# Kernel optimization log

Hardware: AMD Instinct MI355X
Metric: run time of the kernel (lower is better)

Reference implementation:

```python
import jax, jax.numpy as jnp
import numpy as np

N, T, CIN = 40000, 32, 8
VW = 64          # back_voxelwise_channels
P = 16           # v2b_maxvoxels (voxels stacked per BEV cell)
BEV_H, BEV_W = 496, 432
EPS = 1e-5


def _bn(key, shape):
    # returns stacked (gamma, beta, running_mean, running_var) along axis -2
    k1, k2, k3 = jax.random.split(key, 3)
    g = 1.0 + 0.1 * jax.random.normal(k1, shape, jnp.float32)
    b = 0.1 * jax.random.normal(k2, shape, jnp.float32)
    m = 0.1 * jax.random.normal(k3, shape, jnp.float32)
    v = jnp.ones(shape, jnp.float32)
    return jnp.stack([g, b, m, v], axis=-2)


def setup_inputs() -> dict:
    key = jax.random.key(0)
    ks = jax.random.split(key, 20)
    features = jax.random.normal(ks[0], (N, T, CIN), jnp.float32)
    cy = jax.random.randint(ks[1], (N, 1), 0, BEV_H)
    cx = jax.random.randint(ks[2], (N, 1), 0, BEV_W)
    coors = jnp.concatenate([cy, cx], axis=1).astype(jnp.int32)
    num_voxels = jax.random.randint(ks[3], (N,), 1, T + 1).astype(jnp.int32)

    def w(k, o, i):
        return jax.random.normal(k, (o, i), jnp.float32) / float(np.sqrt(i))

    return dict(
        features=features, coors=coors, num_voxels=num_voxels,
        vfe1_W=w(ks[4], 8, CIN), vfe1_bn=_bn(ks[5], (8,)),
        vfe2_W=w(ks[6], 32, 16), vfe2_bn=_bn(ks[7], (32,)),
        vfe3_W=w(ks[8], 64, 64), vfe3_bn=_bn(ks[9], (64,)),
        vfe4_W=w(ks[10], 64, 64), vfe4_bn=_bn(ks[11], (64,)),
        bfe1_W=jax.random.normal(ks[12], (16, P, P), jnp.float32) / float(np.sqrt(P)),
        bfe1_bn=_bn(ks[13], (16, P)),
        bfe2_W=jax.random.normal(ks[14], (16, 2, P), jnp.float32) / float(np.sqrt(P)),
        bfe2_bn=_bn(ks[15], (16, 2)),
        bfe3_W=w(ks[16], 128, 128), bfe3_bn=_bn(ks[17], (128,)),
    )


def _forward(features, vfe1_W, vfe1_bn, vfe2_W, vfe2_bn, vfe3_W, vfe3_bn,
             vfe4_W, vfe4_bn, bfe1_W, bfe1_bn, bfe2_W, bfe2_bn, bfe3_W, bfe3_bn,
             coors, num_voxels):
    n, t = features.shape[0], features.shape[1]
    f32 = features.dtype
    mask = (jnp.arange(t)[None, :] < num_voxels[:, None]).astype(f32)[..., None]  # [N,T,1]

    def fe(x, W, bn):  # Linear (no bias) + BatchNorm1d (eval) + Mish
        g, b, m, v = bn
        y = x @ W.T
        y = (y - m) * jax.lax.rsqrt(v + EPS) * g + b
        return y * jnp.tanh(jax.nn.softplus(y))

    def vfe(x, W, bn):  # pointwise FE, max-pool over points, concat
        p = fe(x, W, bn)
        agg = jnp.max(p, axis=1, keepdims=True)
        return jnp.concatenate([p, jnp.broadcast_to(agg, p.shape)], axis=2)

    x1 = vfe(features, vfe1_W, vfe1_bn)           # [N,T,16]
    x2 = vfe(x1, vfe2_W, vfe2_bn) * mask          # [N,T,64]
    x3 = fe(x2, vfe3_W, vfe3_bn)
    x4 = fe(x3, vfe4_W, vfe4_bn) * mask + x2
    voxelwise = jnp.max(x4, axis=1)               # [N,64]

    # ---- voxel2bev: group voxels by BEV cell, stack up to P per cell ----
    cell = coors[:, 0] * BEV_W + coors[:, 1]                         # [N]
    ucell, inv = jnp.unique(cell, return_inverse=True, size=n, fill_value=BEV_H * BEV_W)
    order = jnp.argsort(inv)                                          # stable
    inv_sorted = inv[order]
    pos_sorted = jnp.arange(n) - jnp.searchsorted(inv_sorted, inv_sorted, side='left')
    slot = jnp.zeros(n, jnp.int32).at[order].set(pos_sorted.astype(jnp.int32))
    row = jnp.where(slot < P, inv, n)                                 # overflow -> dropped
    bevs = jnp.zeros((n, P, VW), f32).at[row, jnp.minimum(slot, P - 1)].set(
        voxelwise, mode='drop')                                       # [N,P,64]
    counts = jax.ops.segment_sum(jnp.ones(n, jnp.int32), inv, num_segments=n)
    numv = jnp.minimum(counts, P)
    bevcoors = jnp.stack([ucell // BEV_W, ucell % BEV_W], axis=1)     # [N,2]

    # ---- 16 grouped FE stacks over the slot dimension ----
    x0 = bevs.transpose(0, 2, 1).reshape(n, 16, 4, P)                 # [N,16,4,P]
    m2 = (jnp.arange(P)[None, :] < numv[:, None]).astype(f32)[:, None, None, :]
    y = jnp.einsum('ngip,gqp->ngiq', x0, bfe1_W)                      # [N,16,4,P]
    g1, b1, m1, v1 = (bfe1_bn[None, :, i, None, :] for i in range(4))
    y = (y - m1) * jax.lax.rsqrt(v1 + EPS) * g1 + b1
    y = y * jnp.tanh(jax.nn.softplus(y)) * m2
    z = jnp.einsum('ngip,gcp->ngic', y, bfe2_W)                       # [N,16,4,2]
    g2, b2, m2b, v2 = (bfe2_bn[None, :, i, None, :] for i in range(4))
    z = (z - m2b) * jax.lax.rsqrt(v2 + EPS) * g2 + b2
    z = z * jnp.tanh(jax.nn.softplus(z))
    # torch cat along dim=-1 then view -> layout [N, 4, 16, 2] flattened
    x17 = z.transpose(0, 2, 1, 3).reshape(n, 128)
    x18 = fe(x17, bfe3_W, bfe3_bn)
    x19 = fe(x18, bfe3_W, bfe3_bn)   # original applies bfe3 twice (bfe4 unused)

    bevmap = jnp.zeros((BEV_H, BEV_W, 128), f32).at[
        bevcoors[:, 0], bevcoors[:, 1]].set(x19, mode='drop')
    return bevmap.transpose(2, 1, 0)                                  # [128, W, H]


def reference(features, coors, num_voxels, vfe1_W, vfe1_bn, vfe2_W, vfe2_bn,
              vfe3_W, vfe3_bn, vfe4_W, vfe4_bn, bfe1_W, bfe1_bn, bfe2_W, bfe2_bn,
              bfe3_W, bfe3_bn):
    return _forward(features, vfe1_W, vfe1_bn, vfe2_W, vfe2_bn, vfe3_W, vfe3_bn,
                    vfe4_W, vfe4_bn, bfe1_W, bfe1_bn, bfe2_W, bfe2_bn,
                    bfe3_W, bfe3_bn, coors, num_voxels)
```

## Files before the change

kernel.cpp:

```cpp
#include <hip/hip_runtime.h>

#define BEVW 432
#define BEVH 496
#define NCELL (BEVW*BEVH)
#define NVOX  40000
#define EPSB  1e-5f

typedef float f32x2 __attribute__((ext_vector_type(2)));
typedef float f32x4 __attribute__((ext_vector_type(4)));
typedef unsigned int u32x4 __attribute__((ext_vector_type(4)));
typedef short bf16x8 __attribute__((ext_vector_type(8)));

#define REP8_0(M)  M(0) M(1) M(2) M(3) M(4) M(5) M(6) M(7)
#define REP8_8(M)  M(8) M(9) M(10) M(11) M(12) M(13) M(14) M(15)
#define REP8_16(M) M(16) M(17) M(18) M(19) M(20) M(21) M(22) M(23)
#define REP8_24(M) M(24) M(25) M(26) M(27) M(28) M(29) M(30) M(31)
#define REP16_0(M)  REP8_0(M)  REP8_8(M)
#define REP32_0(M) REP16_0(M) REP8_16(M) REP8_24(M)


__device__ __forceinline__ float mishf(float y) {
    float e = __expf(fminf(y, 40.f));
    float n = e * (e + 2.f);
    return y * n * __builtin_amdgcn_rcpf(n + 2.f);
}

template <int CTRL>
__device__ __forceinline__ float dppmaxf(float a) {
    int p = __builtin_amdgcn_update_dpp(0, __float_as_int(a), CTRL, 0xF, 0xF, true);
    return fmaxf(a, __int_as_float(p));
}
#define WMAX32(a) { \
    a = dppmaxf<0xB1>(a); \
    a = dppmaxf<0x4E>(a); \
    a = dppmaxf<0x141>(a); \
    a = dppmaxf<0x140>(a); \
    a = fmaxf(a, __int_as_float(__builtin_amdgcn_ds_swizzle(__float_as_int(a), 0x401F))); }

__device__ __forceinline__ bf16x8 mkbf8(uint a, uint b, uint c, uint d) {
    u32x4 t = {a, b, c, d};
    return __builtin_bit_cast(bf16x8, t);
}

__device__ __forceinline__ uint splitbf(float x) {
    uint ux = __float_as_uint(x);
    uint rh = (ux + 0x7FFFu + ((ux >> 16) & 1u)) & 0xFFFF0000u;
    float lof = x - __uint_as_float(rh);
    uint ul = __float_as_uint(lof);
    uint rl = (ul + 0x7FFFu + ((ul >> 16) & 1u)) >> 16;
    return (rh >> 16) | (rl << 16);
}

__global__ __launch_bounds__(256) void setup_kernel(
    const float* __restrict__ vbn1, const float* __restrict__ vbn2,
    const float* __restrict__ vbn3, const float* __restrict__ vbn4,
    const float* __restrict__ bbn1, const float* __restrict__ bbn2,
    const float* __restrict__ bbn3, const float* __restrict__ W4,
    float* __restrict__ fold, ushort* __restrict__ w4fh, ushort* __restrict__ w4fl)
{
    int tid = threadIdx.x;
    if (tid < 8)  { float s = vbn1[tid]/sqrtf(vbn1[24+tid]+EPSB);  fold[tid]      = s; fold[8+tid]   = vbn1[8+tid]  - vbn1[16+tid]*s; }
    if (tid < 32) { float s = vbn2[tid]/sqrtf(vbn2[96+tid]+EPSB);  fold[16+tid]   = s; fold[48+tid]  = vbn2[32+tid] - vbn2[64+tid]*s; }
    if (tid < 64) { float s = vbn3[tid]/sqrtf(vbn3[192+tid]+EPSB); fold[80+tid]   = s; fold[144+tid] = vbn3[64+tid] - vbn3[128+tid]*s; }
    if (tid < 64) { float s = vbn4[tid]/sqrtf(vbn4[192+tid]+EPSB); fold[208+tid]  = s; fold[272+tid] = vbn4[64+tid] - vbn4[128+tid]*s; }
    if (tid < 128){ float s = bbn3[tid]/sqrtf(bbn3[384+tid]+EPSB); fold[336+tid]  = s; fold[464+tid] = bbn3[128+tid]- bbn3[256+tid]*s; }
    { int g = tid >> 4, q = tid & 15;
      const float* b = bbn1 + g*64;
      float s = b[q]/sqrtf(b[48+q]+EPSB);
      fold[592+tid] = s; fold[848+tid] = b[16+q] - b[32+q]*s; }
    if (tid < 32) { int g = tid >> 1, c = tid & 1;
      const float* b = bbn2 + g*8;
      float s = b[c]/sqrtf(b[6+c]+EPSB);
      fold[1104+tid] = s; fold[1136+tid] = b[2+c] - b[4+c]*s; }

    for (int i = tid; i < 4096; i += 256) {
        int j = i & 7, ln = (i >> 3) & 63, nt = (i >> 9) & 3, kc = i >> 11;
        int n = (ln & 15) + nt*16;
        int k = kc*32 + (ln >> 4)*8 + j;
        float val = W4[n*64 + k];
        uint ux = __float_as_uint(val);
        uint rh = (ux + 0x7FFFu + ((ux >> 16) & 1u)) & 0xFFFF0000u;
        float lof = val - __uint_as_float(rh);
        uint ul = __float_as_uint(lof);
        uint rl = (ul + 0x7FFFu + ((ul >> 16) & 1u)) >> 16;
        w4fh[i] = (ushort)(rh >> 16);
        w4fl[i] = (ushort)rl;
    }
}

#define PAIRS(M) M(0,0,1) M(1,2,3) M(2,4,5) M(3,6,7) M(4,8,9) M(5,10,11) \
  M(6,12,13) M(7,14,15) M(8,16,17) M(9,18,19) M(10,20,21) M(11,22,23) \
  M(12,24,25) M(13,26,27) M(14,28,29) M(15,30,31)

#define MF3(D, AH, AL, BH, BL) \
    D = __builtin_amdgcn_mfma_f32_16x16x32_bf16(AL, BH, D, 0, 0, 0); \
    D = __builtin_amdgcn_mfma_f32_16x16x32_bf16(AH, BL, D, 0, 0, 0); \
    D = __builtin_amdgcn_mfma_f32_16x16x32_bf16(AH, BH, D, 0, 0, 0);

__global__ __launch_bounds__(256, 3) void vfe_kernel(
    const float* __restrict__ feat, const int* __restrict__ coors,
    const int* __restrict__ nvx,
    const float* __restrict__ W1, const float* __restrict__ W2,
    const float* __restrict__ W3,
    const ushort* __restrict__ w4fh, const ushort* __restrict__ w4fl,
    const float* __restrict__ fold,
    float* __restrict__ voxelwise, int* __restrict__ cnt,
    int* __restrict__ list, int* __restrict__ nact, int* __restrict__ act)
{
    __shared__ char ldsbuf[4*8704];
    int tid = threadIdx.x;
    int lane = tid & 63;
    int wv = tid >> 6;
    int quad = lane >> 4;
    int v = blockIdx.x * 8 + (tid >> 5);
    int vA = blockIdx.x * 8 + 2*wv;
    int t = tid & 31;
    uint*  x3w  = (uint*)(ldsbuf + wv*8704);
    float* xw   = (float*)x3w;
    float* aggL = (float*)(ldsbuf + wv*8704 + 8448);

    const float* fp = feat + (v*32 + t)*8;
    float4 fa = *(const float4*)fp;
    float4 fb = *(const float4*)(fp+4);
    int numv = nvx[v];
    float maskf = (t < numv) ? 1.f : 0.f;

#define D1(o) float x1_##o; float m1_##o;
    REP8_0(D1)
#undef D1
#define FE1(o) { const float* w = W1 + (o)*8; \
    float ya = fa.x*w[0] + fa.y*w[1]; float yb = fa.z*w[2] + fa.w*w[3]; \
    float yc = fb.x*w[4] + fb.y*w[5]; float yd = fb.z*w[6] + fb.w*w[7]; \
    float yy = ((ya+yb)+(yc+yd)) * fold[(o)] + fold[8+(o)]; \
    x1_##o = mishf(yy); }
    REP8_0(FE1)
#undef FE1
#define P1(o) { float a = x1_##o; WMAX32(a); m1_##o = a; }
    REP8_0(P1)
#undef P1

    f32x2 x1p_0 = {x1_0,x1_1}, x1p_1 = {x1_2,x1_3}, x1p_2 = {x1_4,x1_5}, x1p_3 = {x1_6,x1_7};
    f32x2 m1p_0 = {m1_0,m1_1}, m1p_1 = {m1_2,m1_3}, m1p_2 = {m1_4,m1_5}, m1p_3 = {m1_6,m1_7};

#define D2(o) float x2_##o; float agg_##o;
    REP32_0(D2)
#undef D2
#define FE2(o) { const f32x2* wp = (const f32x2*)(W2 + (o)*16); \
    f32x2 sa = x1p_0*wp[0]; sa += x1p_1*wp[1]; \
    f32x2 sb = x1p_2*wp[2]; sb += x1p_3*wp[3]; \
    f32x2 sc = m1p_0*wp[4]; sc += m1p_1*wp[5]; \
    f32x2 sd = m1p_2*wp[6]; sd += m1p_3*wp[7]; \
    sa += sb; sc += sd; sa += sc; \
    float yy = (sa.x + sa.y) * fold[16+(o)] + fold[48+(o)]; \
    x2_##o = mishf(yy); }
    REP32_0(FE2)
#undef FE2
#define P2(o) { float a = x2_##o; WMAX32(a); agg_##o = a; }
    REP32_0(P2)
#undef P2

#define PX(i,a,b) f32x2 x2p_##i = {x2_##a, x2_##b}; f32x2 aggp_##i = {agg_##a, agg_##b};
    PAIRS(PX)
#undef PX

    const f32x2* wap = (const f32x2*)(W3 + t*64 + 32);
    const f32x2* wbp = (const f32x2*)(W3 + (t+32)*64 + 32);
    f32x2 yp1 = {0.f,0.f}, yp2 = {0.f,0.f};
#define YG(i) yp1 += aggp_##i * wap[i]; yp2 += aggp_##i * wbp[i];
    REP16_0(YG)
#undef YG
    float yagg1 = yp1.x + yp1.y, yagg2 = yp2.x + yp2.y;

    f32x2 maskp = {maskf, maskf};
#define MSK(i) x2p_##i *= maskp; aggp_##i *= maskp;
    REP16_0(MSK)
#undef MSK

    if (t == 0) {
        float* ag = aggL + (lane >> 5)*32;
#define AGW(i) ag[2*(i)] = aggp_##i.x; ag[2*(i)+1] = aggp_##i.y;
        REP16_0(AGW)
#undef AGW
    }

    int nA = __shfl(numv, 0);
    int nB = __shfl(numv, 32);

#define DD(i) f32x4 d_##i = {0.f,0.f,0.f,0.f};
    REP16_0(DD)
#undef DD

    for (int kc = 0; kc < 2; kc++) {
        float ysrc = kc ? yagg2 : yagg1;
        for (int o = 0; o < 32; o++) {
            int og = kc*32 + o;
            const f32x2* wp = (const f32x2*)(W3 + og*64);
            f32x2 s0 = x2p_0*wp[0];  s0 += x2p_1*wp[1];  s0 += x2p_2*wp[2];  s0 += x2p_3*wp[3];
            f32x2 s1 = x2p_4*wp[4];  s1 += x2p_5*wp[5];  s1 += x2p_6*wp[6];  s1 += x2p_7*wp[7];
            f32x2 s2 = x2p_8*wp[8];  s2 += x2p_9*wp[9];  s2 += x2p_10*wp[10]; s2 += x2p_11*wp[11];
            f32x2 s3 = x2p_12*wp[12]; s3 += x2p_13*wp[13]; s3 += x2p_14*wp[14]; s3 += x2p_15*wp[15];
            s0 += s1; s2 += s3; s0 += s2;
            float ya = __shfl(ysrc, o, 32);
            float yy = (s0.x + s0.y) + maskf * ya;
            yy = yy * fold[80+og] + fold[144+og];
            x3w[lane*33 + o] = splitbf(mishf(yy));
        }
        __syncthreads();

        const uint4* bh = (const uint4*)w4fh + (kc*4)*64 + lane;
        const uint4* bl = (const uint4*)w4fl + (kc*4)*64 + lane;

#define MFNT(D, nt) { \
    uint4 h = bh[(nt)*64]; uint4 l = bl[(nt)*64]; \
    bf16x8 Bh = mkbf8(h.x,h.y,h.z,h.w); bf16x8 Bl = mkbf8(l.x,l.y,l.z,l.w); \
    MF3(D, Ah, Al, Bh, Bl) }

#define DOMT(mt, D0, D1, D2, D3) { \
    int aoff = ((lane & 15) + 16*(mt))*33 + quad*8; \
    uint u0 = x3w[aoff+0], u1 = x3w[aoff+1], u2 = x3w[aoff+2], u3 = x3w[aoff+3]; \
    uint u4 = x3w[aoff+4], u5 = x3w[aoff+5], u6 = x3w[aoff+6], u7 = x3w[aoff+7]; \
    bf16x8 Ah = mkbf8(__builtin_amdgcn_perm(u1,u0,0x05040100), __builtin_amdgcn_perm(u3,u2,0x05040100), \
                      __builtin_amdgcn_perm(u5,u4,0x05040100), __builtin_amdgcn_perm(u7,u6,0x05040100)); \
    bf16x8 Al = mkbf8(__builtin_amdgcn_perm(u1,u0,0x07060302), __builtin_amdgcn_perm(u3,u2,0x07060302), \
                      __builtin_amdgcn_perm(u5,u4,0x07060302), __builtin_amdgcn_perm(u7,u6,0x07060302)); \
    MFNT(d_##D0, 0) MFNT(d_##D1, 1) MFNT(d_##D2, 2) MFNT(d_##D3, 3) }

        DOMT(0, 0, 1, 2, 3)
        DOMT(1, 4, 5, 6, 7)
        DOMT(2, 8, 9, 10, 11)
        DOMT(3, 12, 13, 14, 15)
#undef DOMT
#undef MFNT
        __syncthreads();
    }

#define XWR(i) xw[lane*33 + 2*(i)] = x2p_##i.x; xw[lane*33 + 2*(i)+1] = x2p_##i.y;
    REP16_0(XWR)
#undef XWR
    __syncthreads();

    int c0 = lane & 15;
    float s0f = fold[208+c0],    t0f = fold[272+c0];
    float s1f = fold[208+16+c0], t1f = fold[272+16+c0];
    float s2f = fold[208+32+c0], t2f = fold[272+32+c0];
    float s3f = fold[208+48+c0], t3f = fold[272+48+c0];
    float rA2 = aggL[c0],      rA3 = aggL[16+c0];
    float rB2 = aggL[32+c0],   rB3 = aggL[48+c0];
    float pA0=-3.4e38f, pA1=-3.4e38f, pA2=-3.4e38f, pA3=-3.4e38f;
    float pB0=-3.4e38f, pB1=-3.4e38f, pB2=-3.4e38f, pB3=-3.4e38f;

#define FTP(D, mt, nt, SS, TT, PV) { \
    int nv = ((mt) >> 1) ? nB : nA; \
    int rf = quad*4 + 16*(mt); \
    int rt = quad*4 + 16*((mt)&1); \
    int cb = c0 + 16*(nt); \
    float m0=(rt+0<nv)?1.f:0.f, m1=(rt+1<nv)?1.f:0.f, m2=(rt+2<nv)?1.f:0.f, m3=(rt+3<nv)?1.f:0.f; \
    float y0 = mishf(D.x*SS + TT)*m0 + xw[(rf+0)*33 + cb]; \
    float y1 = mishf(D.y*SS + TT)*m1 + xw[(rf+1)*33 + cb]; \
    float y2 = mishf(D.z*SS + TT)*m2 + xw[(rf+2)*33 + cb]; \
    float y3 = mishf(D.w*SS + TT)*m3 + xw[(rf+3)*33 + cb]; \
    PV = fmaxf(PV, fmaxf(fmaxf(y0,y1), fmaxf(y2,y3))); }

#define FTA(D, mt, nt, SS, TT, AG, PV) { \
    int nv = ((mt) >> 1) ? nB : nA; \
    int rt = quad*4 + 16*((mt)&1); \
    float m0=(rt+0<nv)?1.f:0.f, m1=(rt+1<nv)?1.f:0.f, m2=(rt+2<nv)?1.f:0.f, m3=(rt+3<nv)?1.f:0.f; \
    float y0 = (mishf(D.x*SS + TT) + AG)*m0; \
    float y1 = (mishf(D.y*SS + TT) + AG)*m1; \
    float y2 = (mishf(D.z*SS + TT) + AG)*m2; \
    float y3 = (mishf(D.w*SS + TT) + AG)*m3; \
    PV = fmaxf(PV, fmaxf(fmaxf(y0,y1), fmaxf(y2,y3))); }

    FTP(d_0, 0, 0, s0f, t0f, pA0)  FTP(d_1, 0, 1, s1f, t1f, pA1)
    FTA(d_2, 0, 2, s2f, t2f, rA2, pA2)  FTA(d_3, 0, 3, s3f, t3f, rA3, pA3)
    FTP(d_4, 1, 0, s0f, t0f, pA0)  FTP(d_5, 1, 1, s1f, t1f, pA1)
    FTA(d_6, 1, 2, s2f, t2f, rA2, pA2)  FTA(d_7, 1, 3, s3f, t3f, rA3, pA3)
    FTP(d_8, 2, 0, s0f, t0f, pB0)  FTP(d_9, 2, 1, s1f, t1f, pB1)
    FTA(d_10, 2, 2, s2f, t2f, rB2, pB2)  FTA(d_11, 2, 3, s3f, t3f, rB3, pB3)
    FTP(d_12, 3, 0, s0f, t0f, pB0)  FTP(d_13, 3, 1, s1f, t1f, pB1)
    FTA(d_14, 3, 2, s2f, t2f, rB2, pB2)  FTA(d_15, 3, 3, s3f, t3f, rB3, pB3)
#undef FTP
#undef FTA

#define RED(p) p = fmaxf(p, __shfl_xor(p, 16)); p = fmaxf(p, __shfl_xor(p, 32));
    RED(pA0) RED(pA1) RED(pA2) RED(pA3) RED(pB0) RED(pB1) RED(pB2) RED(pB3)
#undef RED

    if (quad == 0) {
        float* vwA = voxelwise + vA*64;
        vwA[c0] = pA0; vwA[c0+16] = pA1; vwA[c0+32] = pA2; vwA[c0+48] = pA3;
        float* vwB = voxelwise + (vA+1)*64;
        vwB[c0] = pB0; vwB[c0+16] = pB1; vwB[c0+32] = pB2; vwB[c0+48] = pB3;
    }

    if (t == 0) {
        int cell = coors[v*2] * BEVW + coors[v*2+1];
        int pos = atomicAdd(&cnt[cell], 1);
        if (pos < 16) list[cell*16 + pos] = v;
        if (pos == 0) { int k = atomicAdd(nact, 1); act[k] = cell; }
    }
}

__global__ __launch_bounds__(256) void bfe_front(
    const int* __restrict__ nact, const int* __restrict__ act,
    const int* __restrict__ cnt, const int* __restrict__ list,
    const float* __restrict__ voxelwise,
    const float* __restrict__ W1g, const float* __restrict__ W2g,
    const float* __restrict__ fold, float* __restrict__ x17g)
{
    int n_act = *nact;
    int aidx = blockIdx.x * 4 + (threadIdx.x >> 6);
    if (aidx >= n_act) return;

    int lane = threadIdx.x & 63;
    int g = lane >> 2, ii = lane & 3;
    int cell = act[aidx];
    int numv = min(cnt[cell], 16);

    int myidx = (lane < numv) ? list[cell*16 + lane] : (0x40000000 + lane);
    int rank = 0;
    for (int j = 0; j < numv; j++) { int vj = __shfl(myidx, j); rank += (vj < myidx) ? 1 : 0; }
    if (lane >= numv) rank = lane;
    int sorted = __builtin_amdgcn_ds_permute(rank << 2, myidx);

#define YD(q) float y_##q = 0.f;
    REP16_0(YD)
#undef YD
    for (int p = 0; p < numv; p++) {
        int sv = __shfl(sorted, p);
        float val = voxelwise[sv*64 + lane];
        const float* w = W1g + g*256 + p;
#define BF1(q) y_##q += val * w[(q)*16];
        REP16_0(BF1)
#undef BF1
    }
#define BN1(q) { float yy = y_##q * fold[592 + g*16 + (q)] + fold[848 + g*16 + (q)]; \
    yy = mishf(yy); y_##q = ((q) < numv) ? yy : 0.f; }
    REP16_0(BN1)
#undef BN1

    float z0 = 0.f, z1 = 0.f;
#define BF2(p) z0 += y_##p * W2g[g*32 + (p)]; z1 += y_##p * W2g[g*32 + 16 + (p)];
    REP16_0(BF2)
#undef BF2
    z0 = mishf(z0 * fold[1104 + g*2 + 0] + fold[1136 + g*2 + 0]);
    z1 = mishf(z1 * fold[1104 + g*2 + 1] + fold[1136 + g*2 + 1]);

    int k0 = ii*32 + g*2;
    *(float2*)(x17g + aidx*128 + k0) = make_float2(z0, z1);
}

__global__ __launch_bounds__(512, 4) void bfe3_fused(
    const int* __restrict__ nactp, const int* __restrict__ act,
    const float* __restrict__ W3, const float* __restrict__ fold,
    const float* __restrict__ x17g, float* __restrict__ out)
{
    __shared__ float XL[64*128];
    int tid = threadIdx.x;
    int n_act = *nactp;
    int cb = blockIdx.x * 64;

    for (int i = tid; i < 64*32; i += 512) {
        int c = i >> 5, kc = i & 31;
        float4 val = (cb + c < n_act) ? ((const float4*)x17g)[(size_t)(cb+c)*32 + kc]
                                      : make_float4(0.f,0.f,0.f,0.f);
        ((float4*)XL)[c*32 + (kc ^ (c & 31))] = val;
    }
    __syncthreads();

    int wv = __builtin_amdgcn_readfirstlane(tid >> 6);
    int c  = tid & 63;
    int ob = wv * 16;
    int cswz = c & 31;
    const float4* xrow = (const float4*)XL + c*32;
    const float4* W4p = (const float4*)W3;

#define DECLB(q) f32x2 ap_##q = {0.f, 0.f};
#define ACCB(q) { const f32x2* wp_ = (const f32x2*)(W4p + (ob+(q))*32 + kc); \
    ap_##q += xv01 * wp_[0]; ap_##q += xv23 * wp_[1]; }
#define ACTB(q) float a_##q; { float yy = (ap_##q.x + ap_##q.y) * fold[336+ob+(q)] + fold[464+ob+(q)]; a_##q = mishf(yy); }
    {
        REP16_0(DECLB)
        for (int kc = 0; kc < 32; kc++) {
            float4 xv = xrow[kc ^ cswz];
            f32x2 xv01 = {xv.x, xv.y}, xv23 = {xv.z, xv.w};
            REP16_0(ACCB)
        }
        REP16_0(ACTB)
        __syncthreads();
        ((float4*)XL)[c*32 + ((wv*4 + 0) ^ cswz)] = make_float4(a_0,  a_1,  a_2,  a_3);
        ((float4*)XL)[c*32 + ((wv*4 + 1) ^ cswz)] = make_float4(a_4,  a_5,  a_6,  a_7);
        ((float4*)XL)[c*32 + ((wv*4 + 2) ^ cswz)] = make_float4(a_8,  a_9,  a_10, a_11);
        ((float4*)XL)[c*32 + ((wv*4 + 3) ^ cswz)] = make_float4(a_12, a_13, a_14, a_15);
    }
    __syncthreads();

    {
        bool active = (cb + c) < n_act;
        int cell = active ? act[cb + c] : 0;
        int hh = cell / BEVW;
        int ww = cell - hh * BEVW;
        float* op = out + (size_t)ob*NCELL + ww*BEVH + hh;
        const float4* yrow = (const float4*)XL + c*32;
        REP16_0(DECLB)
        for (int kc = 0; kc < 32; kc++) {
            float4 xv = yrow[kc ^ cswz];
            f32x2 xv01 = {xv.x, xv.y}, xv23 = {xv.z, xv.w};
            REP16_0(ACCB)
        }
        REP16_0(ACTB)
        if (active) {
#define STOR(q) op[(q)*NCELL] = a_##q;
            REP16_0(STOR)
#undef STOR
        }
    }
#undef DECLB
#undef ACCB
#undef ACTB
}

extern "C" void kernel_launch(void* const* d_in, const int* in_sizes, int n_in,
                              void* d_out, int out_size, void* d_ws, size_t ws_size,
                              hipStream_t stream) {
    const float* features = (const float*)d_in[0];
    const int*   coors    = (const int*)d_in[1];
    const int*   num_vox  = (const int*)d_in[2];
    const float* vfe1_W   = (const float*)d_in[3];
    const float* vfe1_bn  = (const float*)d_in[4];
    const float* vfe2_W   = (const float*)d_in[5];
    const float* vfe2_bn  = (const float*)d_in[6];
    const float* vfe3_W   = (const float*)d_in[7];
    const float* vfe3_bn  = (const float*)d_in[8];
    const float* vfe4_W   = (const float*)d_in[9];
    const float* vfe4_bn  = (const float*)d_in[10];
    const float* bfe1_W   = (const float*)d_in[11];
    const float* bfe1_bn  = (const float*)d_in[12];
    const float* bfe2_W   = (const float*)d_in[13];
    const float* bfe2_bn  = (const float*)d_in[14];
    const float* bfe3_W   = (const float*)d_in[15];
    const float* bfe3_bn  = (const float*)d_in[16];
    float* out = (float*)d_out;

    char* ws = (char*)d_ws;
    int*    nact      = (int*)ws;
    int*    cnt       = (int*)(ws + 256);
    int*    list      = (int*)(ws + 857600);
    float*  voxelwise = (float*)(ws + 14571008);
    int*    act       = (int*)(ws + 24811008);
    float*  x17g      = (float*)(ws + 24971008);
    float*  fold      = (float*)(ws + 45451008);
    ushort* w4fh      = (ushort*)(ws + 45455680);
    ushort* w4fl      = (ushort*)(ws + 45463872);

    (void)hipMemsetAsync(ws, 0, 857600, stream);
    (void)hipMemsetAsync(d_out, 0, (size_t)out_size * sizeof(float), stream);

    setup_kernel<<<1, 256, 0, stream>>>(vfe1_bn, vfe2_bn, vfe3_bn, vfe4_bn,
                                        bfe1_bn, bfe2_bn, bfe3_bn, vfe4_W,
                                        fold, w4fh, w4fl);
    vfe_kernel<<<NVOX/8, 256, 0, stream>>>(features, coors, num_vox,
                                           vfe1_W, vfe2_W, vfe3_W, w4fh, w4fl, fold,
                                           voxelwise, cnt, list, nact, act);
    bfe_front<<<NVOX/4, 256, 0, stream>>>(nact, act, cnt, list, voxelwise,
                                          bfe1_W, bfe2_W, fold, x17g);
    bfe3_fused<<<(NVOX+63)/64, 512, 0, stream>>>(nact, act, bfe3_W, fold, x17g, out);
}
```

Baseline: 591.2 us.

## Replace output memset and scattered stores with gather-based dense BEV writer

Drops the full-output memset and the strided scatter stores in bfe3. bfe_front now records a cell-to-active-index map, bfe3 writes its results compactly back into x17g, and a new bev_write kernel gathers per cell through the map. It transposes in shared memory and writes every output element once with coalesced stores, zero-filling empty cells. The cost is an extra kernel launch, a memset of the index map, and an in-place overwrite of x17g that relies on each block reading its own rows before writing them.

```diff
diff --git a/kernel.cpp b/kernel.cpp
--- a/kernel.cpp
+++ b/kernel.cpp
@@ -306,7 +306,8 @@
     const int* __restrict__ cnt, const int* __restrict__ list,
     const float* __restrict__ voxelwise,
     const float* __restrict__ W1g, const float* __restrict__ W2g,
-    const float* __restrict__ fold, float* __restrict__ x17g)
+    const float* __restrict__ fold, float* __restrict__ x17g,
+    int* __restrict__ idx)
 {
     int n_act = *nact;
     int aidx = blockIdx.x * 4 + (threadIdx.x >> 6);
@@ -316,6 +317,7 @@
     int g = lane >> 2, ii = lane & 3;
     int cell = act[aidx];
     int numv = min(cnt[cell], 16);
+    if (lane == 0) idx[cell] = aidx;
 
     int myidx = (lane < numv) ? list[cell*16 + lane] : (0x40000000 + lane);
     int rank = 0;
@@ -351,9 +353,9 @@
 }
 
 __global__ __launch_bounds__(512, 4) void bfe3_fused(
-    const int* __restrict__ nactp, const int* __restrict__ act,
+    const int* __restrict__ nactp,
     const float* __restrict__ W3, const float* __restrict__ fold,
-    const float* __restrict__ x17g, float* __restrict__ out)
+    float* __restrict__ x17g)
 {
     __shared__ float XL[64*128];
     int tid = threadIdx.x;
@@ -396,11 +398,6 @@
     __syncthreads();
 
     {
-        bool active = (cb + c) < n_act;
-        int cell = active ? act[cb + c] : 0;
-        int hh = cell / BEVW;
-        int ww = cell - hh * BEVW;
-        float* op = out + (size_t)ob*NCELL + ww*BEVH + hh;
         const float4* yrow = (const float4*)XL + c*32;
         REP16_0(DECLB)
         for (int kc = 0; kc < 32; kc++) {
@@ -409,15 +406,55 @@
             REP16_0(ACCB)
         }
         REP16_0(ACTB)
-        if (active) {
-#define STOR(q) op[(q)*NCELL] = a_##q;
-            REP16_0(STOR)
-#undef STOR
-        }
+        float4* dst = (float4*)(x17g + (size_t)(cb + c)*128 + ob);
+        dst[0] = make_float4(a_0,  a_1,  a_2,  a_3);
+        dst[1] = make_float4(a_4,  a_5,  a_6,  a_7);
+        dst[2] = make_float4(a_8,  a_9,  a_10, a_11);
+        dst[3] = make_float4(a_12, a_13, a_14, a_15);
     }
 #undef DECLB
 #undef ACCB
 #undef ACTB
+}
+
+__global__ __launch_bounds__(512, 2) void bev_write(
+    const int* __restrict__ idx, const float* __restrict__ x19c,
+    float* __restrict__ out)
+{
+    __shared__ float XT[128*65];
+    int bid = blockIdx.x;
+    int cx = bid % BEVW;
+    int cy0 = (bid / BEVW) << 6;
+    int tid = threadIdx.x;
+
+    int cell_l = tid >> 3;
+    int chq = (tid & 7) << 4;
+    int cy = cy0 + cell_l;
+    float4 v0 = make_float4(0.f,0.f,0.f,0.f), v1 = v0, v2 = v0, v3 = v0;
+    if (cy < BEVH) {
+        int ai = idx[cy*BEVW + cx];
+        if (ai >= 0) {
+            const float4* src = (const float4*)(x19c + (size_t)ai*128 + chq);
+            v0 = src[0]; v1 = src[1]; v2 = src[2]; v3 = src[3];
+        }
+    }
+    float* d = XT + chq*65 + cell_l;
+    d[0*65]=v0.x;  d[1*65]=v0.y;  d[2*65]=v0.z;  d[3*65]=v0.w;
+    d[4*65]=v1.x;  d[5*65]=v1.y;  d[6*65]=v1.z;  d[7*65]=v1.w;
+    d[8*65]=v2.x;  d[9*65]=v2.y;  d[10*65]=v2.z; d[11*65]=v2.w;
+    d[12*65]=v3.x; d[13*65]=v3.y; d[14*65]=v3.z; d[15*65]=v3.w;
+    __syncthreads();
+
+    int wv2 = tid >> 6, lane = tid & 63;
+    int cyw = cy0 + lane;
+    if (cyw < BEVH) {
+        float* op = out + cx*BEVH + cyw;
+#pragma unroll
+        for (int k = 0; k < 16; k++) {
+            int c = (wv2 << 4) + k;
+            op[(size_t)c*NCELL] = XT[c*65 + lane];
+        }
+    }
 }
 
 extern "C" void kernel_launch(void* const* d_in, const int* in_sizes, int n_in,
@@ -452,9 +489,10 @@
     float*  fold      = (float*)(ws + 45451008);
     ushort* w4fh      = (ushort*)(ws + 45455680);
     ushort* w4fl      = (ushort*)(ws + 45463872);
+    int*    idx       = (int*)(ws + 45472064);
 
     (void)hipMemsetAsync(ws, 0, 857600, stream);
-    (void)hipMemsetAsync(d_out, 0, (size_t)out_size * sizeof(float), stream);
+    (void)hipMemsetAsync(idx, 0xFF, (size_t)NCELL*4, stream);
 
     setup_kernel<<<1, 256, 0, stream>>>(vfe1_bn, vfe2_bn, vfe3_bn, vfe4_bn,
                                         bfe1_bn, bfe2_bn, bfe3_bn, vfe4_W,
@@ -463,6 +501,7 @@
                                            vfe1_W, vfe2_W, vfe3_W, w4fh, w4fl, fold,
                                            voxelwise, cnt, list, nact, act);
     bfe_front<<<NVOX/4, 256, 0, stream>>>(nact, act, cnt, list, voxelwise,
-                                          bfe1_W, bfe2_W, fold, x17g);
-    bfe3_fused<<<(NVOX+63)/64, 512, 0, stream>>>(nact, act, bfe3_W, fold, x17g, out);
-}
+                                          bfe1_W, bfe2_W, fold, x17g, idx);
+    bfe3_fused<<<(NVOX+63)/64, 512, 0, stream>>>(nact, bfe3_W, fold, x17g);
+    bev_write<<<BEVW*8, 512, 0, stream>>>(idx, x17g, out);
+}
```

After: 560.5 us. 1.05x faster.
